# Kernel optimization log

Hardware: AMD Instinct MI355X
Metric: run time of the kernel (lower is better)

## Reference

```python
import jax, jax.numpy as jnp
import numpy as np

N = 20000
NEG_SLOPE = 0.2


def gatv2_layer(x, src, dst, edge_attr, Wl, bl, Wr, br, We, att, bias, H, C):
    """PyG GATv2Conv: add self-loops (edge_attr fill='mean'), gather-score-softmax-aggregate."""
    n = x.shape[0]
    E = src.shape[0]
    # --- add self loops, self-loop edge_attr = mean of incoming edge_attr per node ---
    ea_sum = jax.ops.segment_sum(edge_attr, dst, num_segments=n)
    deg = jax.ops.segment_sum(jnp.ones((E, 1), x.dtype), dst, num_segments=n)
    ea_loop = ea_sum / jnp.maximum(deg, 1.0)
    loop = jnp.arange(n)
    src_a = jnp.concatenate([src, loop])
    dst_a = jnp.concatenate([dst, loop])
    ea = jnp.concatenate([edge_attr, ea_loop], axis=0)
    # --- linear projections ---
    xl = (x @ Wl + bl).reshape(n, H, C)   # source-side features
    xr = (x @ Wr + br).reshape(n, H, C)   # target-side features
    e = (ea @ We).reshape(-1, H, C)       # edge features
    # --- per-edge GATv2 attention score ---
    m = xl[src_a] + xr[dst_a] + e                          # [E', H, C]
    s = jnp.sum(jax.nn.leaky_relu(m, NEG_SLOPE) * att, -1)  # [E', H]
    # --- softmax over incoming edges of each target node ---
    smax = jax.ops.segment_max(s, dst_a, num_segments=n)
    ex = jnp.exp(s - smax[dst_a])
    denom = jax.ops.segment_sum(ex, dst_a, num_segments=n)
    alpha = ex / (denom[dst_a] + 1e-16)                    # [E', H]
    # --- aggregate messages (alpha * x_l[src]) ---
    out = jax.ops.segment_sum(alpha[..., None] * xl[src_a], dst_a, num_segments=n)
    return out.reshape(n, H * C) + bias


def setup_inputs() -> dict:
    key = jax.random.key(0)
    ks = jax.random.split(key, 20)
    F, HID, H1, A = 128, 32, 8, 128
    E = 640000
    d = {}
    d["x"] = jax.random.normal(ks[0], (N, F), jnp.float32)
    d["edge_index"] = jax.random.randint(ks[1], (2, E), 0, N, jnp.int32).astype(jnp.int64)
    d["edge_attr"] = jax.random.normal(ks[2], (E, 1), jnp.float32)
    # layer 1 params (in=F, out=HID, heads=H1)
    d["W1l"] = jax.random.normal(ks[3], (F, H1 * HID), jnp.float32) * 0.05
    d["b1l"] = jnp.zeros((H1 * HID,), jnp.float32)
    d["W1r"] = jax.random.normal(ks[4], (F, H1 * HID), jnp.float32) * 0.05
    d["b1r"] = jnp.zeros((H1 * HID,), jnp.float32)
    d["We1"] = jax.random.normal(ks[5], (1, H1 * HID), jnp.float32) * 0.05
    d["att1"] = jax.random.normal(ks[6], (H1, HID), jnp.float32) * 0.05
    d["bias1"] = jnp.zeros((H1 * HID,), jnp.float32)
    # layer 2 params (in=H1*HID, out=A, heads=1)
    d["W2l"] = jax.random.normal(ks[7], (H1 * HID, A), jnp.float32) * 0.05
    d["b2l"] = jnp.zeros((A,), jnp.float32)
    d["W2r"] = jax.random.normal(ks[8], (H1 * HID, A), jnp.float32) * 0.05
    d["b2r"] = jnp.zeros((A,), jnp.float32)
    d["We2"] = jax.random.normal(ks[9], (1, A), jnp.float32) * 0.05
    d["att2"] = jax.random.normal(ks[10], (1, A), jnp.float32) * 0.05
    d["bias2"] = jnp.zeros((A,), jnp.float32)
    d["alpha"] = jnp.array(0.0, jnp.float32)
    return d


def reference(x, edge_index, edge_attr, W1l, b1l, W1r, b1r, We1, att1, bias1,
              W2l, b2l, W2r, b2r, We2, att2, bias2, alpha):
    src, dst = edge_index[0], edge_index[1]
    h = jax.nn.relu(gatv2_layer(x, src, dst, edge_attr, W1l, b1l, W1r, b1r,
                                We1, att1, bias1, H=8, C=32))
    h = jax.nn.relu(gatv2_layer(h, src, dst, edge_attr, W2l, b2l, W2r, b2r,
                                We2, att2, bias2, H=1, C=128))
    pooled = jnp.mean(h, axis=0, keepdims=True)  # global_mean_pool, single graph -> [1, A]
    return jax.nn.softmax(pooled, axis=1), jax.nn.sigmoid(alpha)
```

## Files before the change

kernel.cpp:

```cpp
#include <hip/hip_runtime.h>
#include <math.h>

#define NEG_SLOPE 0.2f
#define LOG2E 1.4426950408889634f

typedef __attribute__((ext_vector_type(8))) short short8;
typedef __attribute__((ext_vector_type(4))) float f32x4;
typedef __attribute__((ext_vector_type(2))) float v2f;

__device__ __forceinline__ int imin(int a, int b) { return a < b ? a : b; }

__device__ __forceinline__ unsigned int f2bf(float f) {
    unsigned int u = __float_as_uint(f);
    return (u + 0x7fffu + ((u >> 16) & 1u)) >> 16;
}
__device__ __forceinline__ float fast_exp2(float x) {
#if __has_builtin(__builtin_amdgcn_exp2f)
    return __builtin_amdgcn_exp2f(x);
#else
    return exp2f(x);
#endif
}
__device__ __forceinline__ unsigned char f2fp8(float v) {
    return (unsigned char)(__builtin_amdgcn_cvt_pk_fp8_f32(v, v, 0, false) & 0xff);
}
template <int CTRL>
__device__ __forceinline__ float dpp_add(float v) {
    int t = __builtin_amdgcn_update_dpp(0, __float_as_int(v), CTRL, 0xF, 0xF, true);
    return v + __int_as_float(t);
}

__global__ void fused_prep(const int* __restrict__ ei, const float* __restrict__ ea,
                           unsigned long long* __restrict__ hist, int E,
                           const float* __restrict__ x, unsigned short* __restrict__ xb, int nF4,
                           const float* __restrict__ W1l, const float* __restrict__ W1r,
                           const float* __restrict__ W2l, const float* __restrict__ W2r,
                           const float* __restrict__ b1l, const float* __restrict__ b1r,
                           const float* __restrict__ b2l, const float* __restrict__ b2r,
                           unsigned short* __restrict__ Wt1, unsigned short* __restrict__ Wt2,
                           float* __restrict__ b1cat, float* __restrict__ b2cat,
                           int F, int HC1, int HC2) {
    int i = blockIdx.x * blockDim.x + threadIdx.x;
    if (i < E) {
        int d = ei[E + i];
        long long fx = (long long)__float2int_rn(ea[i] * 65536.0f);
        unsigned long long v = ((unsigned long long)fx << 32) | 1ull;
        atomicAdd(&hist[(size_t)d * 8], v);
        return;
    }
    int j = i - E;
    if (j < nF4) {
        float4 v = ((const float4*)x)[j];
        uint2 r;
        r.x = f2bf(v.x) | (f2bf(v.y) << 16);
        r.y = f2bf(v.z) | (f2bf(v.w) << 16);
        ((uint2*)xb)[j] = r;
        return;
    }
    int k = j - nF4;
    int S1 = F * HC1, S2 = HC1 * HC2;
    if (k < S1) {
        int kk = k / HC1, nn = k - kk * HC1;
        Wt1[(size_t)nn * F + kk] = (unsigned short)f2bf(W1l[k]);
    } else if (k < 2 * S1) {
        int m = k - S1;
        int kk = m / HC1, nn = m - kk * HC1;
        Wt1[(size_t)(HC1 + nn) * F + kk] = (unsigned short)f2bf(W1r[m]);
    } else if (k < 2 * S1 + S2) {
        int m = k - 2 * S1;
        int kk = m / HC2, nn = m - kk * HC2;
        Wt2[(size_t)nn * HC1 + kk] = (unsigned short)f2bf(W2l[m]);
    } else if (k < 2 * S1 + 2 * S2) {
        int m = k - 2 * S1 - S2;
        int kk = m / HC2, nn = m - kk * HC2;
        Wt2[(size_t)(HC2 + nn) * HC1 + kk] = (unsigned short)f2bf(W2r[m]);
    } else if (k < 2 * S1 + 2 * S2 + 2 * HC1) {
        int m = k - 2 * S1 - 2 * S2;
        b1cat[m] = (m < HC1) ? b1l[m] : b1r[m - HC1];
    } else if (k < 2 * S1 + 2 * S2 + 2 * HC1 + 2 * HC2) {
        int m = k - 2 * S1 - 2 * S2 - 2 * HC1;
        b2cat[m] = (m < HC2) ? b2l[m] : b2r[m - HC2];
    }
}

__global__ void scan_a(const unsigned long long* __restrict__ hist, int* __restrict__ bsum, int n) {
    __shared__ int wred[4];
    int base = blockIdx.x * 1024;
    int tid = threadIdx.x;
    int s = 0;
#pragma unroll
    for (int k = 0; k < 4; ++k) {
        int i = base + tid + k * 256;
        if (i < n) s += (int)(hist[(size_t)i * 8] & 0xffffffffull);
    }
#pragma unroll
    for (int off = 32; off > 0; off >>= 1) s += __shfl_xor(s, off, 64);
    if ((tid & 63) == 0) wred[tid >> 6] = s;
    __syncthreads();
    if (tid == 0) bsum[blockIdx.x] = wred[0] + wred[1] + wred[2] + wred[3];
}

__global__ void scan_c(const unsigned long long* __restrict__ hist,
                       const int* __restrict__ bsum, int* __restrict__ row_ptr,
                       int* __restrict__ wptr_pad, float* __restrict__ ea_loop,
                       int n, int B) {
    __shared__ int wtot[4];
    __shared__ int sh_base;
    int tid = threadIdx.x;
    int wid = tid >> 6, lane = tid & 63;
    int i0 = blockIdx.x * 1024 + tid * 4;
    int dcnt[4]; float esum[4];
#pragma unroll
    for (int k = 0; k < 4; ++k) {
        if (i0 + k < n) {
            unsigned long long h = hist[(size_t)(i0 + k) * 8];
            dcnt[k] = (int)(h & 0xffffffffull);
            esum[k] = (float)((int)(h >> 32)) * (1.0f / 65536.0f);
        } else { dcnt[k] = 0; esum[k] = 0.0f; }
    }
    int tsum = dcnt[0] + dcnt[1] + dcnt[2] + dcnt[3];
    int s = tsum;
#pragma unroll
    for (int off = 1; off < 64; off <<= 1) {
        int t = __shfl_up(s, off, 64);
        if (lane >= off) s += t;
    }
    if (lane == 63) wtot[wid] = s;
    if (tid < 64) {
        int v   = (tid < B) ? bsum[tid] : 0;
        int pre = (tid < (int)blockIdx.x) ? v : 0;
        int tot = v;
#pragma unroll
        for (int off = 32; off > 0; off >>= 1) {
            pre += __shfl_xor(pre, off, 64);
            tot += __shfl_xor(tot, off, 64);
        }
        if (tid == 0) {
            sh_base = pre;
            if (blockIdx.x == 0) row_ptr[n] = tot;
        }
    }
    __syncthreads();
    int wpre = 0;
#pragma unroll
    for (int k = 0; k < 4; ++k) if (k < wid) wpre += wtot[k];
    int pre = sh_base + wpre + (s - tsum);
    if (i0 < n) {
        int4 e;
        e.x = pre;
        e.y = pre + dcnt[0];
        e.z = e.y + dcnt[1];
        e.w = e.z + dcnt[2];
        *(int4*)(row_ptr + i0) = e;
        int ev[4] = { e.x, e.y, e.z, e.w };
        float4 el;
        el.x = esum[0] / fmaxf((float)dcnt[0], 1.0f);
        el.y = esum[1] / fmaxf((float)dcnt[1], 1.0f);
        el.z = esum[2] / fmaxf((float)dcnt[2], 1.0f);
        el.w = esum[3] / fmaxf((float)dcnt[3], 1.0f);
        *(float4*)(ea_loop + i0) = el;
#pragma unroll
        for (int k = 0; k < 4; ++k) wptr_pad[(size_t)(i0 + k) * 16] = ev[k];
    }
}

__global__ void edge_scatter(const int* __restrict__ ei, const float* __restrict__ ea,
                             int* __restrict__ wptr_pad, int2* __restrict__ spk, int E) {
    int e = blockIdx.x * blockDim.x + threadIdx.x;
    if (e < E) {
        int d = ei[E + e];
        int pos = atomicAdd(&wptr_pad[(size_t)d * 16], 1);
        spk[pos] = make_int2(ei[e], __float_as_int(ea[e]));
    }
}

template <bool OUT_FP8>
__global__ void __launch_bounds__(256)
gemm_bf16(const unsigned short* __restrict__ A, const unsigned short* __restrict__ Bt,
          const float* __restrict__ bias, void* __restrict__ Cv,
          int M, int N, int K) {
    __shared__ __attribute__((aligned(16))) unsigned short As[64 * 40];
    __shared__ __attribute__((aligned(16))) unsigned short Bs[64 * 40];
    int tid  = threadIdx.x;
    int wave = tid >> 6, lane = tid & 63;
    int m0 = blockIdx.x * 64, n0 = blockIdx.y * 64;
    int row = tid >> 2, kg = (tid & 3) * 8;

    f32x4 acc[4] = {};
    for (int kk = 0; kk < K; kk += 32) {
        int gm = m0 + row;
        uint4 av;
        if (gm < M) av = *(const uint4*)(A + (size_t)gm * K + kk + kg);
        else        av = make_uint4(0, 0, 0, 0);
        *(uint4*)&As[row * 40 + kg] = av;
        uint4 bv = *(const uint4*)(Bt + (size_t)(n0 + row) * K + kk + kg);
        *(uint4*)&Bs[row * 40 + kg] = bv;
        __syncthreads();
        short8 a = *(const short8*)&As[(wave * 16 + (lane & 15)) * 40 + (lane >> 4) * 8];
#pragma unroll
        for (int g = 0; g < 4; ++g) {
            short8 b = *(const short8*)&Bs[(g * 16 + (lane & 15)) * 40 + (lane >> 4) * 8];
            acc[g] = __builtin_amdgcn_mfma_f32_16x16x32_bf16(a, b, acc[g], 0, 0, 0);
        }
        __syncthreads();
    }
#pragma unroll
    for (int g = 0; g < 4; ++g) {
        int col = n0 + g * 16 + (lane & 15);
        float bs = bias[col];
#pragma unroll
        for (int r = 0; r < 4; ++r) {
            int grow = m0 + wave * 16 + (lane >> 4) * 4 + r;
            if (grow < M) {
                float val = acc[g][r] + bs;
                if constexpr (OUT_FP8) {
                    ((unsigned char*)Cv)[(size_t)grow * N + col] = f2fp8(val);
                } else {
                    ((unsigned short*)Cv)[(size_t)grow * N + col] = (unsigned short)f2bf(val);
                }
            }
        }
    }
}

template <int NV>
__device__ __forceinline__ void ld_row(float* r, const float* p) {
    if constexpr (NV == 4) {
        float4 t = *(const float4*)p;
        r[0] = t.x; r[1] = t.y; r[2] = t.z; r[3] = t.w;
    } else {
        float2 t = *(const float2*)p;
        r[0] = t.x; r[1] = t.y;
    }
}
template <int NV>
__device__ __forceinline__ unsigned int ld_fp8(const unsigned char* __restrict__ base, int off) {
    if constexpr (NV == 4) return *(const unsigned int*)(base + off);
    else                   return (unsigned int)(*(const unsigned short*)(base + off));
}
template <int NV>
__device__ __forceinline__ void unp_fp8(unsigned int u, float* xf) {
    v2f p0 = __builtin_amdgcn_cvt_pk_f32_fp8(u, false);
    xf[0] = p0.x; xf[1] = p0.y;
    if constexpr (NV == 4) {
        v2f p1 = __builtin_amdgcn_cvt_pk_f32_fp8(u, true);
        xf[2] = p1.x; xf[3] = p1.y;
    }
}
template <int G>
__device__ __forceinline__ float grp_reduce(float vs) {
    vs = dpp_add<0xB1>(vs);
    vs = dpp_add<0x4E>(vs);
    vs = dpp_add<0x141>(vs);
    if constexpr (G >= 16) vs = dpp_add<0x140>(vs);
    if constexpr (G >= 32) {
        int t = __builtin_amdgcn_ds_swizzle(__float_as_int(vs), 0x401F);
        vs += __int_as_float(t);
    }
    if constexpr (G >= 64) vs += __shfl_xor(vs, 32, 64);
    return vs;
}

template <int HC, int STRIDE, int C, int OUT_MODE>
__global__ void __launch_bounds__(256)
gat_agg(const unsigned char* __restrict__ xlr,
        const float* __restrict__ We, const float* __restrict__ att,
        const float* __restrict__ bias,
        const int* __restrict__ row_ptr, const int2* __restrict__ spk,
        const float* __restrict__ ea_loop,
        void* __restrict__ out, int n) {
    constexpr int NV = HC / 64;
    constexpr int G  = C / NV;
    int wave = threadIdx.x >> 6;
    int lane = threadIdx.x & 63;
    int node = blockIdx.x * 4 + wave;
    if (node >= n) return;
    int laneoff = lane * NV;

    float xr_r[NV], We_r[NV], att6[NV], att4[NV], o[NV];
    unp_fp8<NV>(ld_fp8<NV>(xlr + (size_t)node * STRIDE + HC, laneoff), xr_r);
    ld_row<NV>(We_r, We + laneoff);
    {
        float att_r[NV];
        ld_row<NV>(att_r, att + laneoff);
#pragma unroll
        for (int j = 0; j < NV; ++j) {
            att6[j] = 0.6f * LOG2E * att_r[j];
            att4[j] = 0.4f * LOG2E * att_r[j];
        }
    }
#pragma unroll
    for (int j = 0; j < NV; ++j) o[j] = 0.0f;

    int start = __builtin_amdgcn_readfirstlane(row_ptr[node]);
    int end   = __builtin_amdgcn_readfirstlane(row_ptr[node + 1]);
    float ea_l = ea_loop[node];
    float l = 0.0f;

    auto process = [&](unsigned int xu, float w) {
        float xf[NV];
        unp_fp8<NV>(xu, xf);
        float vs = 0.0f;
#pragma unroll
        for (int j = 0; j < NV; ++j) {
            float mm = xf[j] + fmaf(w, We_r[j], xr_r[j]);
            vs = fmaf(att6[j], mm, vs);
            vs = fmaf(att4[j], fabsf(mm), vs);
        }
        vs = grp_reduce<G>(vs);
        float pr = fast_exp2(vs);
        l += pr;
#pragma unroll
        for (int j = 0; j < NV; ++j) o[j] = fmaf(pr, xf[j], o[j]);
    };

    process(ld_fp8<NV>(xlr + (size_t)node * STRIDE, laneoff), ea_l);

    int cnt = end - start;
    for (int b0 = 0; b0 < cnt; b0 += 64) {
        int rem = imin(64, cnt - b0);
        int idx = start + b0 + lane;
        int idxc = imin(idx, end - 1);
        int2 pv = spk[idxc];

        auto rl = [&](int j) {
            int s = __builtin_amdgcn_readlane(pv.x, j);
            return ld_fp8<NV>(xlr + (size_t)s * STRIDE, laneoff);
        };
        auto rw = [&](int j) {
            return __int_as_float(__builtin_amdgcn_readlane(pv.y, j));
        };

        int rc = rem - 1;
        unsigned int A0 = rl(0),           A1 = rl(imin(1, rc)),
                     A2 = rl(imin(2, rc)), A3 = rl(imin(3, rc));
        float Wa0 = rw(0),            Wa1 = rw(imin(1, rc)),
              Wa2 = rw(imin(2, rc)),  Wa3 = rw(imin(3, rc));

        int j = 0;
        for (; j + 8 <= rem; j += 8) {
            unsigned int B0 = rl(j + 4), B1 = rl(j + 5), B2 = rl(j + 6), B3 = rl(j + 7);
            float Wb0 = rw(j + 4), Wb1 = rw(j + 5), Wb2 = rw(j + 6), Wb3 = rw(j + 7);
            process(A0, Wa0); process(A1, Wa1); process(A2, Wa2); process(A3, Wa3);
            A0 = rl(imin(j + 8, rc));  A1 = rl(imin(j + 9, rc));
            A2 = rl(imin(j + 10, rc)); A3 = rl(imin(j + 11, rc));
            Wa0 = rw(imin(j + 8, rc));  Wa1 = rw(imin(j + 9, rc));
            Wa2 = rw(imin(j + 10, rc)); Wa3 = rw(imin(j + 11, rc));
            process(B0, Wb0); process(B1, Wb1); process(B2, Wb2); process(B3, Wb3);
        }
        int left = rem - j;
        if (left > 0) process(A0, Wa0);
        if (left > 1) process(A1, Wa1);
        if (left > 2) process(A2, Wa2);
        if (left > 3) process(A3, Wa3);
        for (int k = j + 4; k < rem; ++k) process(rl(k), rw(k));
    }

    float inv = 1.0f / (l + 1e-16f);
    float b_r[NV];
    ld_row<NV>(b_r, bias + laneoff);
    float v[NV];
#pragma unroll
    for (int j = 0; j < NV; ++j) v[j] = fmaxf(o[j] * inv + b_r[j], 0.0f);

    if constexpr (OUT_MODE == 0) {
        unsigned short* op = (unsigned short*)out + (size_t)node * HC + laneoff;
        if constexpr (NV == 4) {
            uint2 t;
            t.x = f2bf(v[0]) | (f2bf(v[1]) << 16);
            t.y = f2bf(v[2]) | (f2bf(v[3]) << 16);
            *(uint2*)op = t;
        } else {
            *(unsigned int*)op = f2bf(v[0]) | (f2bf(v[1]) << 16);
        }
    } else {
        float* pacc = (float*)out + (size_t)(blockIdx.x & 255) * 128 + laneoff;
#pragma unroll
        for (int j = 0; j < NV; ++j) atomicAdd(&pacc[j], v[j]);
    }
}

__global__ void __launch_bounds__(1024)
pool_final(const float* __restrict__ partial, int nb,
           const float* __restrict__ alpha_in,
           float* __restrict__ out, int n) {
    __shared__ float acc[8][128];
    __shared__ float red[4];
    int t = threadIdx.x & 127;
    int g = threadIdx.x >> 7;
    float s = 0.0f;
    for (int b = g; b < nb; b += 8) s += partial[b * 128 + t];
    acc[g][t] = s;
    __syncthreads();
    if (threadIdx.x < 128) {
        float tot = 0.0f;
#pragma unroll
        for (int k = 0; k < 8; ++k) tot += acc[k][t];
        float mean = tot / (float)n;
        float mx = mean;
#pragma unroll
        for (int off = 32; off > 0; off >>= 1) mx = fmaxf(mx, __shfl_xor(mx, off, 64));
        if ((t & 63) == 0) red[t >> 6] = mx;
        __syncthreads();
        mx = fmaxf(red[0], red[1]);
        float ex = __expf(mean - mx);
        float sm = ex;
#pragma unroll
        for (int off = 32; off > 0; off >>= 1) sm += __shfl_xor(sm, off, 64);
        if ((t & 63) == 0) red[2 + (t >> 6)] = sm;
        __syncthreads();
        sm = red[2] + red[3];
        out[t] = ex / sm;
        if (t == 0) out[128] = 1.0f / (1.0f + __expf(-alpha_in[0]));
    }
}

extern "C" void kernel_launch(void* const* d_in, const int* in_sizes, int n_in,
                              void* d_out, int out_size, void* d_ws, size_t ws_size,
                              hipStream_t stream) {
    const float* x    = (const float*)d_in[0];
    const int*   ei   = (const int*)d_in[1];
    const float* ea   = (const float*)d_in[2];
    const float* W1l  = (const float*)d_in[3];
    const float* b1l  = (const float*)d_in[4];
    const float* W1r  = (const float*)d_in[5];
    const float* b1r  = (const float*)d_in[6];
    const float* We1  = (const float*)d_in[7];
    const float* att1 = (const float*)d_in[8];
    const float* bias1= (const float*)d_in[9];
    const float* W2l  = (const float*)d_in[10];
    const float* b2l  = (const float*)d_in[11];
    const float* W2r  = (const float*)d_in[12];
    const float* b2r  = (const float*)d_in[13];
    const float* We2  = (const float*)d_in[14];
    const float* att2 = (const float*)d_in[15];
    const float* bias2= (const float*)d_in[16];
    const float* alpha= (const float*)d_in[17];
    float* out = (float*)d_out;

    const int F = 128, HC1 = 256, HC2 = 128;
    const int n = in_sizes[0] / F;
    const int E = in_sizes[1] / 2;
    const int B = (n + 1023) / 1024;

    char* ws = (char*)d_ws;
    size_t off = 0;
    auto alloc = [&](size_t bytes) { size_t p = off; off += (bytes + 255) & ~(size_t)255; return p; };

    unsigned long long* hist = (unsigned long long*)(ws + alloc((size_t)n * 8 * 8));
    int*   row_ptr = (int*)  (ws + alloc((size_t)(n + 1) * 4));
    int*   wptr    = (int*)  (ws + alloc((size_t)n * 16 * 4));
    float* ea_loop = (float*)(ws + alloc((size_t)n * 4));
    int*   bsum    = (int*)  (ws + alloc(64 * 4));
    int2*  spk     = (int2*) (ws + alloc((size_t)E * 8));
    unsigned short* xb   = (unsigned short*)(ws + alloc((size_t)n * F * 2));
    unsigned short* Wt1  = (unsigned short*)(ws + alloc((size_t)F * (2 * HC1) * 2));
    unsigned short* Wt2  = (unsigned short*)(ws + alloc((size_t)HC1 * (2 * HC2) * 2));
    float* b1cat   = (float*)(ws + alloc((size_t)2 * HC1 * 4));
    float* b2cat   = (float*)(ws + alloc((size_t)2 * HC2 * 4));
    unsigned char* xlr1 = (unsigned char*)(ws + alloc((size_t)n * 2 * HC1));
    unsigned short* h1  = (unsigned short*)(ws + alloc((size_t)n * HC1 * 2));
    float* partial = (float*)(ws + alloc((size_t)256 * 128 * 4));
    unsigned char* xlr2 = xlr1;
    const int NB_SLOTS = 256;

    (void)hipMemsetAsync(hist, 0, (size_t)n * 8 * 8, stream);
    (void)hipMemsetAsync(partial, 0, (size_t)NB_SLOTS * 128 * 4, stream);

    int tb = 256;
    {
        int nF4  = n * F / 4;
        int WTOT = 2 * F * HC1 + 2 * HC1 * HC2 + 2 * HC1 + 2 * HC2;
        int total = E + nF4 + WTOT;
        fused_prep<<<(total + tb - 1) / tb, tb, 0, stream>>>(
            ei, ea, hist, E, x, xb, nF4,
            W1l, W1r, W2l, W2r, b1l, b1r, b2l, b2r,
            Wt1, Wt2, b1cat, b2cat, F, HC1, HC2);
    }
    scan_a<<<B, 256, 0, stream>>>(hist, bsum, n);
    scan_c<<<B, 256, 0, stream>>>(hist, bsum, row_ptr, wptr, ea_loop, n, B);
    edge_scatter<<<(E + tb - 1) / tb, tb, 0, stream>>>(ei, ea, wptr, spk, E);

    {
        dim3 grid((n + 63) / 64, (2 * HC1) / 64);
        gemm_bf16<true><<<grid, 256, 0, stream>>>(xb, Wt1, b1cat, xlr1, n, 2 * HC1, F);
    }
    gat_agg<256, 512, 32, 0><<<(n + 3) / 4, 256, 0, stream>>>(
        xlr1, We1, att1, bias1, row_ptr, spk, ea_loop, h1, n);

    {
        dim3 grid((n + 63) / 64, (2 * HC2) / 64);
        gemm_bf16<true><<<grid, 256, 0, stream>>>(h1, Wt2, b2cat, xlr2, n, 2 * HC2, HC1);
    }
    gat_agg<128, 256, 128, 1><<<(n + 3) / 4, 256, 0, stream>>>(
        xlr2, We2, att2, bias2, row_ptr, spk, ea_loop, partial, n);

    pool_final<<<1, 1024, 0, stream>>>(partial, NB_SLOTS, alpha, out, n);
}
```

Baseline: 278.2 us.

## Process two edges per wave in GAT aggregation using half-wave split and packed math

New measurement: 292.2 us. 1.05x slower.

```diff
diff --git a/kernel.cpp b/kernel.cpp
--- a/kernel.cpp
+++ b/kernel.cpp
@@ -223,41 +223,25 @@
     }
 }
 
-template <int NV>
-__device__ __forceinline__ void ld_row(float* r, const float* p) {
-    if constexpr (NV == 4) {
-        float4 t = *(const float4*)p;
-        r[0] = t.x; r[1] = t.y; r[2] = t.z; r[3] = t.w;
-    } else {
-        float2 t = *(const float2*)p;
-        r[0] = t.x; r[1] = t.y;
-    }
-}
-template <int NV>
-__device__ __forceinline__ unsigned int ld_fp8(const unsigned char* __restrict__ base, int off) {
-    if constexpr (NV == 4) return *(const unsigned int*)(base + off);
-    else                   return (unsigned int)(*(const unsigned short*)(base + off));
-}
-template <int NV>
-__device__ __forceinline__ void unp_fp8(unsigned int u, float* xf) {
-    v2f p0 = __builtin_amdgcn_cvt_pk_f32_fp8(u, false);
-    xf[0] = p0.x; xf[1] = p0.y;
-    if constexpr (NV == 4) {
-        v2f p1 = __builtin_amdgcn_cvt_pk_f32_fp8(u, true);
-        xf[2] = p1.x; xf[3] = p1.y;
+template <int NG>
+__device__ __forceinline__ void unp2(uint2 u, v2f* xf) {
+    xf[0] = __builtin_amdgcn_cvt_pk_f32_fp8(u.x, false);
+    xf[1] = __builtin_amdgcn_cvt_pk_f32_fp8(u.x, true);
+    if constexpr (NG == 4) {
+        xf[2] = __builtin_amdgcn_cvt_pk_f32_fp8(u.y, false);
+        xf[3] = __builtin_amdgcn_cvt_pk_f32_fp8(u.y, true);
     }
 }
 template <int G>
-__device__ __forceinline__ float grp_reduce(float vs) {
+__device__ __forceinline__ float grp_reduce32(float vs) {
     vs = dpp_add<0xB1>(vs);
-    vs = dpp_add<0x4E>(vs);
-    vs = dpp_add<0x141>(vs);
+    if constexpr (G >= 4)  vs = dpp_add<0x4E>(vs);
+    if constexpr (G >= 8)  vs = dpp_add<0x141>(vs);
     if constexpr (G >= 16) vs = dpp_add<0x140>(vs);
     if constexpr (G >= 32) {
         int t = __builtin_amdgcn_ds_swizzle(__float_as_int(vs), 0x401F);
         vs += __int_as_float(t);
     }
-    if constexpr (G >= 64) vs += __shfl_xor(vs, 32, 64);
     return vs;
 }
 
@@ -269,114 +253,146 @@
         const int* __restrict__ row_ptr, const int2* __restrict__ spk,
         const float* __restrict__ ea_loop,
         void* __restrict__ out, int n) {
-    constexpr int NV = HC / 64;
+    constexpr int NV = HC / 32;
+    constexpr int NG = NV / 2;
     constexpr int G  = C / NV;
+    constexpr float K23 = 2.0f / 3.0f;
     int wave = threadIdx.x >> 6;
     int lane = threadIdx.x & 63;
     int node = blockIdx.x * 4 + wave;
     if (node >= n) return;
-    int laneoff = lane * NV;
-
-    float xr_r[NV], We_r[NV], att6[NV], att4[NV], o[NV];
-    unp_fp8<NV>(ld_fp8<NV>(xlr + (size_t)node * STRIDE + HC, laneoff), xr_r);
-    ld_row<NV>(We_r, We + laneoff);
+    unsigned int lo32 = (unsigned int)(lane & 31) * NV;
+
+    auto ldd = [&](unsigned int off) -> uint2 {
+        uint2 r;
+        if constexpr (NV == 8) r = *(const uint2*)(xlr + off);
+        else { r.x = *(const unsigned int*)(xlr + off); r.y = 0u; }
+        return r;
+    };
+
+    v2f xr2[NG], We2[NG], att62[NG], o2[NG];
     {
-        float att_r[NV];
-        ld_row<NV>(att_r, att + laneoff);
-#pragma unroll
-        for (int j = 0; j < NV; ++j) {
-            att6[j] = 0.6f * LOG2E * att_r[j];
-            att4[j] = 0.4f * LOG2E * att_r[j];
-        }
-    }
-#pragma unroll
-    for (int j = 0; j < NV; ++j) o[j] = 0.0f;
+        uint2 xru = ldd((unsigned int)node * STRIDE + HC + lo32);
+        unp2<NG>(xru, xr2);
+    }
+#pragma unroll
+    for (int g = 0; g < NG; ++g) {
+        We2[g]   = *(const v2f*)(We  + lo32 + 2 * g);
+        v2f a    = *(const v2f*)(att + lo32 + 2 * g);
+        att62[g] = a * (0.6f * LOG2E);
+        o2[g]    = v2f{0.0f, 0.0f};
+    }
+    float l = 0.0f;
 
     int start = __builtin_amdgcn_readfirstlane(row_ptr[node]);
     int end   = __builtin_amdgcn_readfirstlane(row_ptr[node + 1]);
     float ea_l = ea_loop[node];
-    float l = 0.0f;
-
-    auto process = [&](unsigned int xu, float w) {
-        float xf[NV];
-        unp_fp8<NV>(xu, xf);
-        float vs = 0.0f;
-#pragma unroll
-        for (int j = 0; j < NV; ++j) {
-            float mm = xf[j] + fmaf(w, We_r[j], xr_r[j]);
-            vs = fmaf(att6[j], mm, vs);
-            vs = fmaf(att4[j], fabsf(mm), vs);
-        }
-        vs = grp_reduce<G>(vs);
+
+    auto process = [&](uint2 du, float w, bool maskhi) {
+        v2f xf[NG];
+        unp2<NG>(du, xf);
+        v2f vs2 = v2f{0.0f, 0.0f};
+#pragma unroll
+        for (int g = 0; g < NG; ++g) {
+            v2f t  = We2[g] * w + xr2[g];
+            v2f mm = xf[g] + t;
+            v2f u;
+            u.x = fmaf(fabsf(mm.x), K23, mm.x);
+            u.y = fmaf(fabsf(mm.y), K23, mm.y);
+            vs2 = att62[g] * u + vs2;
+        }
+        float vs = vs2.x + vs2.y;
+        vs = grp_reduce32<G>(vs);
         float pr = fast_exp2(vs);
+        if (maskhi && lane >= 32) pr = 0.0f;
         l += pr;
 #pragma unroll
-        for (int j = 0; j < NV; ++j) o[j] = fmaf(pr, xf[j], o[j]);
+        for (int g = 0; g < NG; ++g) o2[g] = xf[g] * pr + o2[g];
     };
 
-    process(ld_fp8<NV>(xlr + (size_t)node * STRIDE, laneoff), ea_l);
+    process(ldd((unsigned int)node * STRIDE + lo32), ea_l, true);
 
     int cnt = end - start;
     for (int b0 = 0; b0 < cnt; b0 += 64) {
         int rem = imin(64, cnt - b0);
-        int idx = start + b0 + lane;
-        int idxc = imin(idx, end - 1);
+        int idxc = imin(start + b0 + lane, end - 1);
         int2 pv = spk[idxc];
 
-        auto rl = [&](int j) {
-            int s = __builtin_amdgcn_readlane(pv.x, j);
-            return ld_fp8<NV>(xlr + (size_t)s * STRIDE, laneoff);
+        auto ldp = [&](int p) -> uint2 {
+            int sA = __builtin_amdgcn_readlane(pv.x, 2 * p);
+            int sB = __builtin_amdgcn_readlane(pv.x, 2 * p + 1);
+            int s  = (lane < 32) ? sA : sB;
+            return ldd((unsigned int)s * STRIDE + lo32);
         };
-        auto rw = [&](int j) {
-            return __int_as_float(__builtin_amdgcn_readlane(pv.y, j));
+        auto ldw = [&](int p) -> float {
+            int wA = __builtin_amdgcn_readlane(pv.y, 2 * p);
+            int wB = __builtin_amdgcn_readlane(pv.y, 2 * p + 1);
+            return __int_as_float((lane < 32) ? wA : wB);
         };
 
-        int rc = rem - 1;
-        unsigned int A0 = rl(0),           A1 = rl(imin(1, rc)),
-                     A2 = rl(imin(2, rc)), A3 = rl(imin(3, rc));
-        float Wa0 = rw(0),            Wa1 = rw(imin(1, rc)),
-              Wa2 = rw(imin(2, rc)),  Wa3 = rw(imin(3, rc));
-
-        int j = 0;
-        for (; j + 8 <= rem; j += 8) {
-            unsigned int B0 = rl(j + 4), B1 = rl(j + 5), B2 = rl(j + 6), B3 = rl(j + 7);
-            float Wb0 = rw(j + 4), Wb1 = rw(j + 5), Wb2 = rw(j + 6), Wb3 = rw(j + 7);
-            process(A0, Wa0); process(A1, Wa1); process(A2, Wa2); process(A3, Wa3);
-            A0 = rl(imin(j + 8, rc));  A1 = rl(imin(j + 9, rc));
-            A2 = rl(imin(j + 10, rc)); A3 = rl(imin(j + 11, rc));
-            Wa0 = rw(imin(j + 8, rc));  Wa1 = rw(imin(j + 9, rc));
-            Wa2 = rw(imin(j + 10, rc)); Wa3 = rw(imin(j + 11, rc));
-            process(B0, Wb0); process(B1, Wb1); process(B2, Wb2); process(B3, Wb3);
-        }
-        int left = rem - j;
-        if (left > 0) process(A0, Wa0);
-        if (left > 1) process(A1, Wa1);
-        if (left > 2) process(A2, Wa2);
-        if (left > 3) process(A3, Wa3);
-        for (int k = j + 4; k < rem; ++k) process(rl(k), rw(k));
-    }
-
+        int npair = rem >> 1;
+        if (npair > 0) {
+            int pc = npair - 1;
+            uint2 A0 = ldp(0), A1 = ldp(imin(1, pc));
+            float Wa0 = ldw(0), Wa1 = ldw(imin(1, pc));
+            int p = 0;
+            for (; p + 4 <= npair; p += 4) {
+                uint2 B0 = ldp(p + 2), B1 = ldp(p + 3);
+                float Wb0 = ldw(p + 2), Wb1 = ldw(p + 3);
+                process(A0, Wa0, false); process(A1, Wa1, false);
+                A0 = ldp(imin(p + 4, pc)); A1 = ldp(imin(p + 5, pc));
+                Wa0 = ldw(imin(p + 4, pc)); Wa1 = ldw(imin(p + 5, pc));
+                process(B0, Wb0, false); process(B1, Wb1, false);
+            }
+            int left = npair - p;
+            if (left > 0) process(A0, Wa0, false);
+            if (left > 1) process(A1, Wa1, false);
+            for (int k = p + 2; k < npair; ++k) process(ldp(k), ldw(k), false);
+        }
+        if (rem & 1) {
+            int e = rem - 1;
+            int s = __builtin_amdgcn_readlane(pv.x, e);
+            float w = __int_as_float(__builtin_amdgcn_readlane(pv.y, e));
+            process(ldd((unsigned int)s * STRIDE + lo32), w, true);
+        }
+    }
+
+    l += __shfl_xor(l, 32, 64);
+#pragma unroll
+    for (int g = 0; g < NG; ++g) {
+        o2[g].x += __shfl_xor(o2[g].x, 32, 64);
+        o2[g].y += __shfl_xor(o2[g].y, 32, 64);
+    }
     float inv = 1.0f / (l + 1e-16f);
-    float b_r[NV];
-    ld_row<NV>(b_r, bias + laneoff);
-    float v[NV];
-#pragma unroll
-    for (int j = 0; j < NV; ++j) v[j] = fmaxf(o[j] * inv + b_r[j], 0.0f);
-
-    if constexpr (OUT_MODE == 0) {
-        unsigned short* op = (unsigned short*)out + (size_t)node * HC + laneoff;
-        if constexpr (NV == 4) {
-            uint2 t;
-            t.x = f2bf(v[0]) | (f2bf(v[1]) << 16);
-            t.y = f2bf(v[2]) | (f2bf(v[3]) << 16);
-            *(uint2*)op = t;
+
+    if (lane < 32) {
+        float v[NV];
+#pragma unroll
+        for (int g = 0; g < NG; ++g) {
+            v2f b = *(const v2f*)(bias + lo32 + 2 * g);
+            v[2 * g]     = fmaxf(o2[g].x * inv + b.x, 0.0f);
+            v[2 * g + 1] = fmaxf(o2[g].y * inv + b.y, 0.0f);
+        }
+        if constexpr (OUT_MODE == 0) {
+            unsigned short* op = (unsigned short*)out + (size_t)node * HC + lo32;
+            if constexpr (NV == 8) {
+                uint4 t;
+                t.x = f2bf(v[0]) | (f2bf(v[1]) << 16);
+                t.y = f2bf(v[2]) | (f2bf(v[3]) << 16);
+                t.z = f2bf(v[4]) | (f2bf(v[5]) << 16);
+                t.w = f2bf(v[6]) | (f2bf(v[7]) << 16);
+                *(uint4*)op = t;
+            } else {
+                uint2 t;
+                t.x = f2bf(v[0]) | (f2bf(v[1]) << 16);
+                t.y = f2bf(v[2]) | (f2bf(v[3]) << 16);
+                *(uint2*)op = t;
+            }
         } else {
-            *(unsigned int*)op = f2bf(v[0]) | (f2bf(v[1]) << 16);
-        }
-    } else {
-        float* pacc = (float*)out + (size_t)(blockIdx.x & 255) * 128 + laneoff;
-#pragma unroll
-        for (int j = 0; j < NV; ++j) atomicAdd(&pacc[j], v[j]);
+            float* pacc = (float*)out + (size_t)(blockIdx.x & 255) * 128 + lo32;
+#pragma unroll
+            for (int j = 0; j < NV; ++j) atomicAdd(&pacc[j], v[j]);
+        }
     }
 }
 
```
